# Performance work log

Hardware: AMD Instinct MI355X
Metric: run time of the kernel (lower is better)

Reference implementation:

```python
import jax, jax.numpy as jnp
import numpy as np

N = 131072
IN, HID, OUT = 128, 256, 64
NUM_TASKS = 16
NUM_COPIES = 4
NUM_LAYERS = 3


def setup_inputs() -> dict:
    key = jax.random.key(0)
    ks = jax.random.split(key, 10)
    inputs = jax.random.normal(ks[0], (N, IN), dtype=jnp.float32)
    task_indices = jax.random.randint(ks[1], (N,), 0, NUM_TASKS, dtype=jnp.int32)
    copy_maps = jax.random.randint(ks[2], (NUM_LAYERS, NUM_TASKS), 0, NUM_COPIES, dtype=jnp.int32)
    # per-copy Linear weights, Kaiming-ish scale 1/sqrt(fan_in)
    W0 = jax.random.normal(ks[3], (NUM_COPIES, IN, HID), dtype=jnp.float32) / np.sqrt(IN)
    b0 = jax.random.normal(ks[4], (NUM_COPIES, HID), dtype=jnp.float32) * 0.01
    W1 = jax.random.normal(ks[5], (NUM_COPIES, HID, HID), dtype=jnp.float32) / np.sqrt(HID)
    b1 = jax.random.normal(ks[6], (NUM_COPIES, HID), dtype=jnp.float32) * 0.01
    W2 = jax.random.normal(ks[7], (NUM_COPIES, HID, OUT), dtype=jnp.float32) / np.sqrt(HID)
    b2 = jax.random.normal(ks[8], (NUM_COPIES, OUT), dtype=jnp.float32) * 0.01
    return {"inputs": inputs, "task_indices": task_indices, "copy_maps": copy_maps,
            "W0": W0, "b0": b0, "W1": W1, "b1": b1, "W2": W2, "b2": b2}


def _routed_layer(x, W, b, copy_idx, apply_tanh):
    # x: [N, d_in], W: [C, d_in, d_out], b: [C, d_out], copy_idx: [N]
    # Each token goes through exactly one copy's Linear. Equivalent to the
    # torch sort->per-copy-forward->unsort, expressed as masked accumulation
    # over the small fixed set of copies (avoids data-dependent shapes).
    y = jnp.zeros((x.shape[0], W.shape[2]), dtype=x.dtype)
    for c in range(W.shape[0]):
        mask = (copy_idx == c).astype(x.dtype)[:, None]  # [N, 1]
        y = y + mask * (x @ W[c] + b[c])
    return jnp.tanh(y) if apply_tanh else y


def reference(inputs, task_indices, copy_maps, W0, b0, W1, b1, W2, b2):
    x = inputs
    Ws = (W0, W1, W2)
    bs = (b0, b1, b2)
    for layer in range(NUM_LAYERS):
        copy_idx = copy_maps[layer][task_indices]  # [N] task->copy routing
        x = _routed_layer(x, Ws[layer], bs[layer], copy_idx,
                          apply_tanh=(layer != NUM_LAYERS - 1))
    return x
```

## Files before the change

kernel.cpp:

```cpp
#include <hip/hip_runtime.h>

#define N_TOK 131072
#define TILE 64
#define NT_MAX 2064
#define NBLK 256

typedef __attribute__((ext_vector_type(8))) short s8v;
typedef __attribute__((ext_vector_type(4))) float f4v;
typedef unsigned short ushort_t;

__device__ __forceinline__ unsigned short f2bf(float x) {
    union { float f; unsigned u; } v; v.f = x;
    unsigned r = v.u + 0x7fffu + ((v.u >> 16) & 1u);
    return (unsigned short)(r >> 16);
}

__device__ __forceinline__ unsigned pk2(float a, float b) {
    union { float f; unsigned u; } x, y; x.f = a; y.f = b;
    return __byte_perm(x.u + 0x8000u, y.u + 0x8000u, 0x7632);
}

__device__ __forceinline__ float tanh_fast(float x) {
    float e = __builtin_amdgcn_exp2f(x * 2.8853900817779268f);
    float r = __builtin_amdgcn_rcpf(e + 1.0f);
    return __builtin_fmaf(-2.0f, r, 1.0f);
}

__global__ void prep_hist_kernel(const float* __restrict__ W0, const float* __restrict__ W1,
                                 const float* __restrict__ W2,
                                 ushort_t* __restrict__ W0p, ushort_t* __restrict__ W1p,
                                 ushort_t* __restrict__ W2p,
                                 const int* __restrict__ task, int* __restrict__ blockCounts) {
    if (blockIdx.x < 224) {
        int f = blockIdx.x * 256 + threadIdx.x;
        const float* src; ushort_t* dst; int K, N;
        if (f < 16384)      { src = W0; dst = W0p; K = 128; N = 256; }
        else if (f < 49152) { src = W1; dst = W1p; K = 256; N = 256; f -= 16384; }
        else                { src = W2; dst = W2p; K = 256; N = 64;  f -= 49152; }
        int fpc = (N >> 4) * (K >> 5) * 64;
        int c = f / fpc, r = f % fpc;
        int lane = r & 63;
        int kt = (r >> 6) % (K >> 5);
        int ftile = (r >> 6) / (K >> 5);
        int n = ftile * 16 + (lane & 15);
        int kbase = kt * 32 + (lane >> 4) * 8;
        const float* s = src + (size_t)c * K * N + (size_t)kbase * N + n;
        s8v pk;
#pragma unroll
        for (int j = 0; j < 8; j++) pk[j] = (short)f2bf(s[(size_t)j * N]);
        *reinterpret_cast<s8v*>(dst + ((size_t)(c * fpc + r) << 3)) = pk;
    } else {
        __shared__ int cnt[16];
        int t = threadIdx.x;
        int hb = blockIdx.x - 224;
        if (t < 16) cnt[t] = 0;
        __syncthreads();
        int base = hb * 2048 + t;
#pragma unroll
        for (int i = 0; i < 8; i++) atomicAdd(&cnt[task[base + i * 256]], 1);
        __syncthreads();
        if (t < 16) blockCounts[hb * 16 + t] = cnt[t];
    }
}

__global__ void sort_kernel(const int* __restrict__ task, const int* __restrict__ blockCounts,
                            int* __restrict__ tbaseG, int* __restrict__ perm) {
    __shared__ int cntLds[1024];
    __shared__ int total[16], pref[16], rank[16];
    __shared__ int tokBase[16], tbase[17];
    int t = threadIdx.x, b = blockIdx.x;
    for (int i = t; i < 1024; i += 256) cntLds[i] = blockCounts[i];
    if (t < 16) rank[t] = 0;
    __syncthreads();
    if (t < 16) {
        int tot = 0, pf = 0;
#pragma unroll
        for (int bb = 0; bb < 64; bb++) {
            int v = cntLds[bb * 16 + t];
            tot += v;
            if (bb < b) pf += v;
        }
        total[t] = tot; pref[t] = pf;
    }
    __syncthreads();
    if (t == 0) {
        int tok = 0, tile = 0;
        for (int k = 0; k < 16; k++) {
            tokBase[k] = tok;
            tbase[k] = tile;
            int ntk = (total[k] + TILE - 1) / TILE;
            tok += ntk * TILE;
            tile += ntk;
        }
        tbase[16] = tile;
    }
    __syncthreads();
    if (b == 0) {
        if (t < 17) tbaseG[t] = tbase[t];
        for (int i = t; i < 16 * TILE; i += 256) {
            int k = i >> 6, off = i & (TILE - 1);
            int idx = total[k] + off;
            int lim = ((total[k] + TILE - 1) / TILE) * TILE;
            if (idx < lim) perm[tokBase[k] + idx] = -1;
        }
    }
    int tk[8], my[8];
#pragma unroll
    for (int i = 0; i < 8; i++) {
        int idx = b * 2048 + i * 256 + t;
        tk[i] = task[idx];
        my[i] = atomicAdd(&rank[tk[i]], 1);
    }
#pragma unroll
    for (int i = 0; i < 8; i++) {
        int idx = b * 2048 + i * 256 + t;
        perm[tokBase[tk[i]] + pref[tk[i]] + my[i]] = idx;
    }
}

__launch_bounds__(512, 2)
__global__ void mlp_kernel(const float* __restrict__ x_in,
                           const int* __restrict__ cmap,
                           const float* __restrict__ b0,
                           const float* __restrict__ b1,
                           const float* __restrict__ b2,
                           const ushort_t* __restrict__ W0p,
                           const ushort_t* __restrict__ W1p,
                           const ushort_t* __restrict__ W2p,
                           const int* __restrict__ tbaseG,
                           const int* __restrict__ perm,
                           float* __restrict__ out) {
    __shared__ __align__(16) ushort_t Xb[2][8192];
    __shared__ __align__(16) ushort_t H1[16384];
    __shared__ __align__(16) ushort_t H2[16384];

    int p = blockIdx.x;
    int x = p & 7, s = p >> 3;
    int k = 2 * x + (s >> 4), sub = s & 15;
    int tBeg = tbaseG[k], tEnd = tbaseG[k + 1];
    if (tBeg + sub >= tEnd) return;

    int t = threadIdx.x;
    int c0 = cmap[k], c1 = cmap[16 + k], c2 = cmap[32 + k];

    int w = t >> 6;
    int lane = t & 63;
    int l15 = lane & 15, lq = lane >> 4;
    int mt2 = w & 3, ntb2 = (w >> 2) * 2;

    const ushort_t* Wc0 = W0p + (size_t)c0 * 32768;
    const ushort_t* Wc1 = W1p + (size_t)c1 * 65536;
    const ushort_t* Wc2 = W2p + (size_t)c2 * 16384;

    f4v bv0[2], bv1[2], bv2;
#pragma unroll
    for (int mi = 0; mi < 2; mi++) {
        bv0[mi] = *reinterpret_cast<const f4v*>(b0 + c0 * 256 + (2 * w + mi) * 16 + lq * 4);
        bv1[mi] = *reinterpret_cast<const f4v*>(b1 + c1 * 256 + (2 * w + mi) * 16 + lq * 4);
    }
    bv2 = *reinterpret_cast<const f4v*>(b2 + c2 * 64 + mt2 * 16 + lq * 4);

    int r = t >> 3, q = t & 7;
    int fragid = (r >> 4) * 4 + (q >> 1);
    int lp0 = (r & 15) + 16 * ((q & 1) * 2);
    const float4* xbase = reinterpret_cast<const float4*>(x_in);

    int tile = tBeg + sub;
    {
        int ptok = perm[tile * TILE + r];
        float4 v0 = make_float4(0.f, 0.f, 0.f, 0.f), v1 = v0, v2 = v0, v3 = v0;
        if ((unsigned)ptok < (unsigned)N_TOK) {
            const float4* src = xbase + (size_t)ptok * 32 + q * 4;
            v0 = src[0]; v1 = src[1]; v2 = src[2]; v3 = src[3];
        }
        uint4 pk0, pk1;
        pk0.x = pk2(v0.x, v0.y); pk0.y = pk2(v0.z, v0.w);
        pk0.z = pk2(v1.x, v1.y); pk0.w = pk2(v1.z, v1.w);
        pk1.x = pk2(v2.x, v2.y); pk1.y = pk2(v2.z, v2.w);
        pk1.z = pk2(v3.x, v3.y); pk1.w = pk2(v3.z, v3.w);
        *reinterpret_cast<uint4*>(&Xb[0][(fragid * 64 + lp0) << 3]) = pk0;
        *reinterpret_cast<uint4*>(&Xb[0][(fragid * 64 + lp0 + 16) << 3]) = pk1;
    }
    __syncthreads();

    int cur = 0;
    for (; tile < tEnd; tile += 16) {
        int ntile = tile + 16;
        bool hasNext = ntile < tEnd;

        float4 a0 = make_float4(0.f, 0.f, 0.f, 0.f), a1 = a0, a2 = a0, a3 = a0;
        if (hasNext) {
            int ptok = perm[ntile * TILE + r];
            if ((unsigned)ptok < (unsigned)N_TOK) {
                const float4* src = xbase + (size_t)ptok * 32 + q * 4;
                a0 = src[0]; a1 = src[1]; a2 = src[2]; a3 = src[3];
            }
        }

        {
            f4v acc[2][4];
#pragma unroll
            for (int mi = 0; mi < 2; mi++)
#pragma unroll
                for (int nt = 0; nt < 4; nt++)
                    acc[mi][nt] = bv0[mi];
#pragma unroll
            for (int kt = 0; kt < 4; kt++) {
                s8v wa[2], xb[4];
#pragma unroll
                for (int mi = 0; mi < 2; mi++)
                    wa[mi] = *reinterpret_cast<const s8v*>(Wc0 + ((((2 * w + mi) * 4 + kt) * 64 + lane) << 3));
#pragma unroll
                for (int nt = 0; nt < 4; nt++)
                    xb[nt] = *reinterpret_cast<const s8v*>(&Xb[cur][((nt * 4 + kt) * 64 + lane) << 3]);
#pragma unroll
                for (int mi = 0; mi < 2; mi++)
#pragma unroll
                    for (int nt = 0; nt < 4; nt++)
                        acc[mi][nt] = __builtin_amdgcn_mfma_f32_16x16x32_bf16(wa[mi], xb[nt], acc[mi][nt], 0, 0, 0);
            }
#pragma unroll
            for (int mi = 0; mi < 2; mi++) {
                int ft = 2 * w + mi;
                int kt_h = ft >> 1;
                int lanep = l15 + 16 * ((ft & 1) * 2 + (lq >> 1));
                int j0 = (lq & 1) * 4;
#pragma unroll
                for (int nt = 0; nt < 4; nt++) {
                    float t0 = tanh_fast(acc[mi][nt][0]);
                    float t1 = tanh_fast(acc[mi][nt][1]);
                    float t2 = tanh_fast(acc[mi][nt][2]);
                    float t3 = tanh_fast(acc[mi][nt][3]);
                    uint2 pk; pk.x = pk2(t0, t1); pk.y = pk2(t2, t3);
                    *reinterpret_cast<uint2*>(&H1[(((nt * 8 + kt_h) * 64 + lanep) << 3) + j0]) = pk;
                }
            }
        }
        __syncthreads();

        {
            f4v acc[2][4];
#pragma unroll
            for (int mi = 0; mi < 2; mi++)
#pragma unroll
                for (int nt = 0; nt < 4; nt++)
                    acc[mi][nt] = bv1[mi];
#pragma unroll
            for (int kt = 0; kt < 8; kt++) {
                s8v wa[2], xb[4];
#pragma unroll
                for (int mi = 0; mi < 2; mi++)
                    wa[mi] = *reinterpret_cast<const s8v*>(Wc1 + ((((2 * w + mi) * 8 + kt) * 64 + lane) << 3));
#pragma unroll
                for (int nt = 0; nt < 4; nt++)
                    xb[nt] = *reinterpret_cast<const s8v*>(&H1[((nt * 8 + kt) * 64 + lane) << 3]);
#pragma unroll
                for (int mi = 0; mi < 2; mi++)
#pragma unroll
                    for (int nt = 0; nt < 4; nt++)
                        acc[mi][nt] = __builtin_amdgcn_mfma_f32_16x16x32_bf16(wa[mi], xb[nt], acc[mi][nt], 0, 0, 0);
            }
            if (hasNext) {
                uint4 pk0, pk1;
                pk0.x = pk2(a0.x, a0.y); pk0.y = pk2(a0.z, a0.w);
                pk0.z = pk2(a1.x, a1.y); pk0.w = pk2(a1.z, a1.w);
                pk1.x = pk2(a2.x, a2.y); pk1.y = pk2(a2.z, a2.w);
                pk1.z = pk2(a3.x, a3.y); pk1.w = pk2(a3.z, a3.w);
                *reinterpret_cast<uint4*>(&Xb[cur ^ 1][(fragid * 64 + lp0) << 3]) = pk0;
                *reinterpret_cast<uint4*>(&Xb[cur ^ 1][(fragid * 64 + lp0 + 16) << 3]) = pk1;
            }
#pragma unroll
            for (int mi = 0; mi < 2; mi++) {
                int ft = 2 * w + mi;
                int kt_h = ft >> 1;
                int lanep = l15 + 16 * ((ft & 1) * 2 + (lq >> 1));
                int j0 = (lq & 1) * 4;
#pragma unroll
                for (int nt = 0; nt < 4; nt++) {
                    float t0 = tanh_fast(acc[mi][nt][0]);
                    float t1 = tanh_fast(acc[mi][nt][1]);
                    float t2 = tanh_fast(acc[mi][nt][2]);
                    float t3 = tanh_fast(acc[mi][nt][3]);
                    uint2 pk; pk.x = pk2(t0, t1); pk.y = pk2(t2, t3);
                    *reinterpret_cast<uint2*>(&H2[(((nt * 8 + kt_h) * 64 + lanep) << 3) + j0]) = pk;
                }
            }
        }
        __syncthreads();

        {
            int tok0 = perm[tile * TILE + ntb2 * 16 + l15];
            int tok1 = perm[tile * TILE + (ntb2 + 1) * 16 + l15];
            f4v acc[2];
            acc[0] = bv2; acc[1] = bv2;
#pragma unroll
            for (int kt = 0; kt < 8; kt++) {
                s8v wa = *reinterpret_cast<const s8v*>(Wc2 + (((mt2 * 8 + kt) * 64 + lane) << 3));
#pragma unroll
                for (int e = 0; e < 2; e++) {
                    s8v xb = *reinterpret_cast<const s8v*>(&H2[(((ntb2 + e) * 8 + kt) * 64 + lane) << 3]);
                    acc[e] = __builtin_amdgcn_mfma_f32_16x16x32_bf16(wa, xb, acc[e], 0, 0, 0);
                }
            }
#pragma unroll
            for (int e = 0; e < 2; e++) {
                int tok = e ? tok1 : tok0;
                if ((unsigned)tok < (unsigned)N_TOK) {
                    float4 o;
                    o.x = acc[e][0]; o.y = acc[e][1]; o.z = acc[e][2]; o.w = acc[e][3];
                    *reinterpret_cast<float4*>(out + (size_t)tok * 64 + mt2 * 16 + lq * 4) = o;
                }
            }
        }
        __syncthreads();
        cur ^= 1;
    }
}

extern "C" void kernel_launch(void* const* d_in, const int* in_sizes, int n_in,
                              void* d_out, int out_size, void* d_ws, size_t ws_size,
                              hipStream_t stream) {
    const float* inputs = (const float*)d_in[0];
    const int*   task   = (const int*)d_in[1];
    const int*   cmap   = (const int*)d_in[2];
    const float* W0     = (const float*)d_in[3];
    const float* b0     = (const float*)d_in[4];
    const float* W1     = (const float*)d_in[5];
    const float* b1     = (const float*)d_in[6];
    const float* W2     = (const float*)d_in[7];
    const float* b2     = (const float*)d_in[8];
    float* out = (float*)d_out;

    char* ws = (char*)d_ws;
    int* blockCounts = (int*)(ws + 0);
    int* tbaseG      = (int*)(ws + 4096);
    int* perm        = (int*)(ws + 4224);
    ushort_t* W0p    = (ushort_t*)(ws + 532608);
    ushort_t* W1p    = (ushort_t*)(ws + 794752);
    ushort_t* W2p    = (ushort_t*)(ws + 1319040);

    prep_hist_kernel<<<288, 256, 0, stream>>>(W0, W1, W2, W0p, W1p, W2p, task, blockCounts);
    sort_kernel<<<64, 256, 0, stream>>>(task, blockCounts, tbaseG, perm);
    mlp_kernel<<<NBLK, 512, 0, stream>>>(inputs, cmap, b0, b1, b2,
                                         W0p, W1p, W2p, tbaseG, perm, out);
}
```

Before: 162.5 us.

## Fuse weight prep, sort and MLP into one cooperative kernel with grid syncs

```diff
diff --git a/kernel.cpp b/kernel.cpp
--- a/kernel.cpp
+++ b/kernel.cpp
@@ -1,4 +1,7 @@
 #include <hip/hip_runtime.h>
+#include <hip/hip_cooperative_groups.h>
+
+namespace cg = cooperative_groups;
 
 #define N_TOK 131072
 #define TILE 64
@@ -26,13 +29,29 @@
     return __builtin_fmaf(-2.0f, r, 1.0f);
 }
 
-__global__ void prep_hist_kernel(const float* __restrict__ W0, const float* __restrict__ W1,
-                                 const float* __restrict__ W2,
-                                 ushort_t* __restrict__ W0p, ushort_t* __restrict__ W1p,
-                                 ushort_t* __restrict__ W2p,
-                                 const int* __restrict__ task, int* __restrict__ blockCounts) {
-    if (blockIdx.x < 224) {
-        int f = blockIdx.x * 256 + threadIdx.x;
+__launch_bounds__(512, 2)
+__global__ void fused_kernel(const float* __restrict__ x_in,
+                             const int* __restrict__ task,
+                             const int* __restrict__ cmap,
+                             const float* __restrict__ W0,
+                             const float* __restrict__ b0,
+                             const float* __restrict__ W1,
+                             const float* __restrict__ b1,
+                             const float* __restrict__ W2,
+                             const float* __restrict__ b2,
+                             ushort_t* W0p, ushort_t* W1p, ushort_t* W2p,
+                             int* blockCounts, int* tbaseG, int* perm,
+                             float* __restrict__ out) {
+    __shared__ __align__(16) ushort_t Xb[2][8192];
+    __shared__ __align__(16) ushort_t H1[16384];
+    __shared__ __align__(16) ushort_t H2[16384];
+
+    cg::grid_group grid = cg::this_grid();
+    int p = blockIdx.x, t = threadIdx.x;
+    int gid = p * 512 + t;
+
+    if (gid < 57344) {
+        int f = gid;
         const float* src; ushort_t* dst; int K, N;
         if (f < 16384)      { src = W0; dst = W0p; K = 128; N = 256; }
         else if (f < 49152) { src = W1; dst = W1p; K = 256; N = 256; f -= 16384; }
@@ -49,98 +68,65 @@
 #pragma unroll
         for (int j = 0; j < 8; j++) pk[j] = (short)f2bf(s[(size_t)j * N]);
         *reinterpret_cast<s8v*>(dst + ((size_t)(c * fpc + r) << 3)) = pk;
-    } else {
-        __shared__ int cnt[16];
-        int t = threadIdx.x;
-        int hb = blockIdx.x - 224;
+    }
+    int myTask = task[gid];
+    {
+        int* cnt = (int*)H1;
         if (t < 16) cnt[t] = 0;
         __syncthreads();
-        int base = hb * 2048 + t;
-#pragma unroll
-        for (int i = 0; i < 8; i++) atomicAdd(&cnt[task[base + i * 256]], 1);
-        __syncthreads();
-        if (t < 16) blockCounts[hb * 16 + t] = cnt[t];
-    }
-}
-
-__global__ void sort_kernel(const int* __restrict__ task, const int* __restrict__ blockCounts,
-                            int* __restrict__ tbaseG, int* __restrict__ perm) {
-    __shared__ int cntLds[1024];
-    __shared__ int total[16], pref[16], rank[16];
-    __shared__ int tokBase[16], tbase[17];
-    int t = threadIdx.x, b = blockIdx.x;
-    for (int i = t; i < 1024; i += 256) cntLds[i] = blockCounts[i];
-    if (t < 16) rank[t] = 0;
-    __syncthreads();
-    if (t < 16) {
-        int tot = 0, pf = 0;
-#pragma unroll
-        for (int bb = 0; bb < 64; bb++) {
-            int v = cntLds[bb * 16 + t];
-            tot += v;
-            if (bb < b) pf += v;
-        }
-        total[t] = tot; pref[t] = pf;
-    }
-    __syncthreads();
-    if (t == 0) {
-        int tok = 0, tile = 0;
-        for (int k = 0; k < 16; k++) {
-            tokBase[k] = tok;
-            tbase[k] = tile;
-            int ntk = (total[k] + TILE - 1) / TILE;
-            tok += ntk * TILE;
-            tile += ntk;
-        }
-        tbase[16] = tile;
-    }
-    __syncthreads();
-    if (b == 0) {
-        if (t < 17) tbaseG[t] = tbase[t];
-        for (int i = t; i < 16 * TILE; i += 256) {
-            int k = i >> 6, off = i & (TILE - 1);
-            int idx = total[k] + off;
-            int lim = ((total[k] + TILE - 1) / TILE) * TILE;
-            if (idx < lim) perm[tokBase[k] + idx] = -1;
-        }
-    }
-    int tk[8], my[8];
-#pragma unroll
-    for (int i = 0; i < 8; i++) {
-        int idx = b * 2048 + i * 256 + t;
-        tk[i] = task[idx];
-        my[i] = atomicAdd(&rank[tk[i]], 1);
-    }
-#pragma unroll
-    for (int i = 0; i < 8; i++) {
-        int idx = b * 2048 + i * 256 + t;
-        perm[tokBase[tk[i]] + pref[tk[i]] + my[i]] = idx;
-    }
-}
-
-__launch_bounds__(512, 2)
-__global__ void mlp_kernel(const float* __restrict__ x_in,
-                           const int* __restrict__ cmap,
-                           const float* __restrict__ b0,
-                           const float* __restrict__ b1,
-                           const float* __restrict__ b2,
-                           const ushort_t* __restrict__ W0p,
-                           const ushort_t* __restrict__ W1p,
-                           const ushort_t* __restrict__ W2p,
-                           const int* __restrict__ tbaseG,
-                           const int* __restrict__ perm,
-                           float* __restrict__ out) {
-    __shared__ __align__(16) ushort_t Xb[2][8192];
-    __shared__ __align__(16) ushort_t H1[16384];
-    __shared__ __align__(16) ushort_t H2[16384];
-
-    int p = blockIdx.x;
+        atomicAdd(&cnt[myTask], 1);
+        __syncthreads();
+        if (t < 16) blockCounts[p * 16 + t] = cnt[t];
+    }
+    grid.sync();
+
+    {
+        int* cLds = (int*)H2;
+        int* sc   = (int*)H1;
+        for (int i = t; i < 4096; i += 512) cLds[i] = blockCounts[i];
+        if (t < 16) sc[32 + t] = 0;
+        __syncthreads();
+        if (t < 16) {
+            int tot = 0, pf = 0;
+            for (int bb = 0; bb < 256; bb++) {
+                int v = cLds[bb * 16 + t];
+                tot += v;
+                if (bb < p) pf += v;
+            }
+            sc[t] = tot; sc[16 + t] = pf;
+        }
+        __syncthreads();
+        if (t == 0) {
+            int tok = 0, tile = 0;
+            for (int k2 = 0; k2 < 16; k2++) {
+                sc[48 + k2] = tok;
+                sc[64 + k2] = tile;
+                int ntk = (sc[k2] + TILE - 1) >> 6;
+                tok += ntk * TILE;
+                tile += ntk;
+            }
+            sc[80] = tile;
+        }
+        __syncthreads();
+        if (p == 0) {
+            if (t < 17) tbaseG[t] = sc[64 + t];
+            for (int i = t; i < 16 * TILE; i += 512) {
+                int k2 = i >> 6, off = i & (TILE - 1);
+                int idx = sc[k2] + off;
+                int lim = ((sc[k2] + TILE - 1) >> 6) << 6;
+                if (idx < lim) perm[sc[48 + k2] + idx] = -1;
+            }
+        }
+        int my = atomicAdd(&sc[32 + myTask], 1);
+        perm[sc[48 + myTask] + sc[16 + myTask] + my] = gid;
+    }
+    grid.sync();
+
     int x = p & 7, s = p >> 3;
     int k = 2 * x + (s >> 4), sub = s & 15;
     int tBeg = tbaseG[k], tEnd = tbaseG[k + 1];
     if (tBeg + sub >= tEnd) return;
 
-    int t = threadIdx.x;
     int c0 = cmap[k], c1 = cmap[16 + k], c2 = cmap[32 + k];
 
     int w = t >> 6;
@@ -160,14 +146,14 @@
     }
     bv2 = *reinterpret_cast<const f4v*>(b2 + c2 * 64 + mt2 * 16 + lq * 4);
 
-    int r = t >> 3, q = t & 7;
-    int fragid = (r >> 4) * 4 + (q >> 1);
-    int lp0 = (r & 15) + 16 * ((q & 1) * 2);
+    int r2 = t >> 3, q = t & 7;
+    int fragid = (r2 >> 4) * 4 + (q >> 1);
+    int lp0 = (r2 & 15) + 16 * ((q & 1) * 2);
     const float4* xbase = reinterpret_cast<const float4*>(x_in);
 
     int tile = tBeg + sub;
     {
-        int ptok = perm[tile * TILE + r];
+        int ptok = perm[tile * TILE + r2];
         float4 v0 = make_float4(0.f, 0.f, 0.f, 0.f), v1 = v0, v2 = v0, v3 = v0;
         if ((unsigned)ptok < (unsigned)N_TOK) {
             const float4* src = xbase + (size_t)ptok * 32 + q * 4;
@@ -190,7 +176,7 @@
 
         float4 a0 = make_float4(0.f, 0.f, 0.f, 0.f), a1 = a0, a2 = a0, a3 = a0;
         if (hasNext) {
-            int ptok = perm[ntile * TILE + r];
+            int ptok = perm[ntile * TILE + r2];
             if ((unsigned)ptok < (unsigned)N_TOK) {
                 const float4* src = xbase + (size_t)ptok * 32 + q * 4;
                 a0 = src[0]; a1 = src[1]; a2 = src[2]; a3 = src[3];
@@ -333,14 +319,19 @@
 
     char* ws = (char*)d_ws;
     int* blockCounts = (int*)(ws + 0);
-    int* tbaseG      = (int*)(ws + 4096);
-    int* perm        = (int*)(ws + 4224);
-    ushort_t* W0p    = (ushort_t*)(ws + 532608);
-    ushort_t* W1p    = (ushort_t*)(ws + 794752);
-    ushort_t* W2p    = (ushort_t*)(ws + 1319040);
-
-    prep_hist_kernel<<<288, 256, 0, stream>>>(W0, W1, W2, W0p, W1p, W2p, task, blockCounts);
-    sort_kernel<<<64, 256, 0, stream>>>(task, blockCounts, tbaseG, perm);
-    mlp_kernel<<<NBLK, 512, 0, stream>>>(inputs, cmap, b0, b1, b2,
-                                         W0p, W1p, W2p, tbaseG, perm, out);
-}
+    int* tbaseG      = (int*)(ws + 16384);
+    int* perm        = (int*)(ws + 16512);
+    ushort_t* W0p    = (ushort_t*)(ws + 544896);
+    ushort_t* W1p    = (ushort_t*)(ws + 807040);
+    ushort_t* W2p    = (ushort_t*)(ws + 1331328);
+
+    void* args[] = {
+        (void*)&inputs, (void*)&task, (void*)&cmap,
+        (void*)&W0, (void*)&b0, (void*)&W1, (void*)&b1, (void*)&W2, (void*)&b2,
+        (void*)&W0p, (void*)&W1p, (void*)&W2p,
+        (void*)&blockCounts, (void*)&tbaseG, (void*)&perm,
+        (void*)&out
+    };
+    hipLaunchCooperativeKernel((const void*)fused_kernel, dim3(NBLK), dim3(512),
+                               args, 0, stream);
+}
```

Result: slower. 249.3 us (+53.4%).
